# Kernel tuning notes

Measured on AMD Instinct MI355X. Metric: run time of the kernel, lower is better.

## Reference

```python
import jax, jax.numpy as jnp
import numpy as np

D_MODEL, HIDDEN, H, NB = 1024, 128, 16, 32
B, L = 4, 4096


def setup_inputs() -> dict:
    key = jax.random.key(0)
    ks = jax.random.split(key, 6)
    theta_path = jax.random.normal(ks[0], (B, L, H, NB), dtype=jnp.float32)
    content_emb = jax.random.normal(ks[1], (B, L, D_MODEL), dtype=jnp.float32)
    # params (log_Pi init 0.0; final linear weight scaled by 0.01, bias 0, as in torch init)
    log_Pi = jnp.zeros((H, NB), dtype=jnp.float32)
    W1 = jax.random.normal(ks[2], (D_MODEL, HIDDEN), dtype=jnp.float32) / np.sqrt(D_MODEL)
    b1 = jnp.zeros((HIDDEN,), dtype=jnp.float32)
    W2 = (jax.random.normal(ks[3], (HIDDEN, H * NB), dtype=jnp.float32) / np.sqrt(HIDDEN)) * 0.01
    b2 = jnp.zeros((H * NB,), dtype=jnp.float32)
    return {"theta_path": theta_path, "content_emb": content_emb,
            "log_Pi": log_Pi, "W1": W1, "b1": b1, "W2": W2, "b2": b2}


def _affine_combine(c1, c2):
    a1, u1 = c1
    a2, u2 = c2
    return a2 * a1, a2 * u1 + u2


def reference(theta_path, content_emb, log_Pi, W1, b1, W2, b2):
    Bx, Lx, Hx, NBx = theta_path.shape
    # log_R_head: Linear -> GELU(exact) -> Linear, then clamp
    h = jax.nn.gelu(content_emb @ W1 + b1, approximate=False)
    log_R = jnp.clip((h @ W2 + b2).reshape(Bx, Lx, Hx, NBx), -5.0, 5.0)
    R = jnp.exp(log_R)
    # wrapped innovation nu = atan2(sin(-theta), cos(-theta))
    nu = jnp.arctan2(jnp.sin(-theta_path), jnp.cos(-theta_path))
    Pi = jnp.exp(log_Pi)[None, None]            # [1,1,H,NB]
    K = Pi / jnp.maximum(Pi + R, 1e-8)
    alpha = 1.0 - K
    u = K * nu
    # affine recurrence d_t = alpha_t * d_{t-1} + u_t, parallel scan over L
    _, d = jax.lax.associative_scan(_affine_combine, (alpha, u), axis=1)
    return theta_path + d, jnp.broadcast_to(Pi, R.shape), K, R
```

## Files before the change

kernel.cpp:

```cpp
#include <hip/hip_runtime.h>
#include <math.h>

#define B_   4
#define L_   4096
#define C_   512
#define DM_  1024
#define HID_ 128
#define M_   (B_*L_)
#define NC_  256
#define CT_  16

typedef __attribute__((ext_vector_type(8))) short short8;
typedef __attribute__((ext_vector_type(4))) float f32x4;

__device__ __forceinline__ unsigned short f2bf(float f) {
  unsigned u = __float_as_uint(f);
  u += 0x7fffu + ((u >> 16) & 1u);
  return (unsigned short)(u >> 16);
}

__device__ __forceinline__ float wrap_neg(float th) {
  return 6.283185307179586f * rintf(th * 0.15915494309189535f) - th;
}

__global__ __launch_bounds__(256) void k_prep(const float* __restrict__ W1,
                                              const float* __restrict__ W2,
                                              unsigned short* __restrict__ W1T,
                                              unsigned short* __restrict__ W2T) {
  int idx = blockIdx.x * 256 + threadIdx.x;
  if (idx < DM_ * HID_) {
    int n = idx >> 10, k = idx & 1023;
    W1T[idx] = f2bf(W1[(size_t)k * HID_ + n]);
  }
  int i2 = idx - DM_ * HID_;
  if (i2 >= 0 && i2 < HID_ * C_) {
    int n = i2 >> 7, k = i2 & 127;
    W2T[i2] = f2bf(W2[(size_t)k * C_ + n]);
  }
}

__global__ __launch_bounds__(512) void k_mega(const float* __restrict__ X,
                                              const unsigned short* __restrict__ W1T,
                                              const float* __restrict__ b1,
                                              const unsigned short* __restrict__ W2T,
                                              const float* __restrict__ b2,
                                              const float* __restrict__ logPi,
                                              const float* __restrict__ theta,
                                              float* __restrict__ out1,
                                              float* __restrict__ out2,
                                              float* __restrict__ out3,
                                              float* __restrict__ Ab,
                                              float* __restrict__ Ub) {
  __shared__ char lds[49152];
  const int tid  = threadIdx.x;
  const int m0   = blockIdx.x * 32;
  const int lane = tid & 63;
  const int wave = tid >> 6;
  const int wr   = wave >> 2;
  const int wc   = wave & 3;
  const int fr   = lane & 15;
  const int kg   = lane >> 4;

  f32x4 acc[2];
  acc[0] = (f32x4){0.f, 0.f, 0.f, 0.f};
  acc[1] = (f32x4){0.f, 0.f, 0.f, 0.f};

#define STAGE1(bufi, k0)                                                           \
  {                                                                                \
    if (tid < 256) {                                                               \
      int row = tid >> 3, k8 = tid & 7;                                            \
      const f32x4* src = (const f32x4*)(X + (size_t)(m0 + row) * DM_ + (k0) + k8 * 8); \
      f32x4 v0 = __builtin_nontemporal_load(src);                                  \
      f32x4 v1 = __builtin_nontemporal_load(src + 1);                              \
      uint4 pk;                                                                    \
      pk.x = f2bf(v0[0]) | ((unsigned)f2bf(v0[1]) << 16);                          \
      pk.y = f2bf(v0[2]) | ((unsigned)f2bf(v0[3]) << 16);                          \
      pk.z = f2bf(v1[0]) | ((unsigned)f2bf(v1[1]) << 16);                          \
      pk.w = f2bf(v1[2]) | ((unsigned)f2bf(v1[3]) << 16);                          \
      *(uint4*)(lds + (bufi) * 4096 + row * 128 + ((k8 ^ (row & 7)) << 4)) = pk;   \
    }                                                                              \
    _Pragma("unroll")                                                              \
    for (int t = 0; t < 2; ++t) {                                                  \
      int c = tid + t * 512;                                                       \
      int n = c >> 3, k8 = c & 7;                                                  \
      uint4 v = *(const uint4*)(W1T + (size_t)n * DM_ + (k0) + k8 * 8);            \
      *(uint4*)(lds + 8192 + (bufi) * 16384 + n * 128 + ((k8 ^ (n & 7)) << 4)) = v;\
    }                                                                              \
  }

  STAGE1(0, 0);
  __syncthreads();
  for (int it = 0; it < 16; ++it) {
    const int cur = it & 1;
    if (it < 15) STAGE1(1 - cur, (it + 1) * 64);
#pragma unroll
    for (int ks = 0; ks < 2; ++ks) {
      int row = wr * 16 + fr;
      short8 a = *(const short8*)(lds + cur * 4096 + row * 128 +
                                  (((ks * 4 + kg) ^ (row & 7)) << 4));
#pragma unroll
      for (int j = 0; j < 2; ++j) {
        int col = wc * 32 + j * 16 + fr;
        short8 b = *(const short8*)(lds + 8192 + cur * 16384 + col * 128 +
                                    (((ks * 4 + kg) ^ (col & 7)) << 4));
        acc[j] = __builtin_amdgcn_mfma_f32_16x16x32_bf16(a, b, acc[j], 0, 0, 0);
      }
    }
    __syncthreads();
  }
#pragma unroll
  for (int j = 0; j < 2; ++j) {
    int col = wc * 32 + j * 16 + fr;
    float bb = b1[col];
#pragma unroll
    for (int r = 0; r < 4; ++r) {
      int row = wr * 16 + kg * 4 + r;
      float x = acc[j][r] + bb;
      float g = 0.5f * x * (1.0f + erff(x * 0.70710678f));
      *(unsigned short*)(lds + 40960 + row * 256 +
                         (((col >> 3) ^ (row & 15)) << 4) + ((col & 7) << 1)) = f2bf(g);
    }
  }

  const int bidx = m0 >> 12;
  const int ch   = ((m0 & 4095) >> 4) + wr;
  const size_t chbase = ((size_t)(bidx * NC_ + ch)) * C_;

#define STAGE2(bufi, nc)                                                           \
  {                                                                                \
    _Pragma("unroll")                                                              \
    for (int t = 0; t < 2; ++t) {                                                  \
      int c = tid + t * 512;                                                       \
      int n = c >> 4, k8 = c & 15;                                                 \
      uint4 v = *(const uint4*)(W2T + (size_t)((nc) * 64 + n) * HID_ + k8 * 8);    \
      *(uint4*)(lds + (bufi) * 16384 + n * 256 + ((k8 ^ (n & 15)) << 4)) = v;      \
    }                                                                              \
  }

  STAGE2(0, 0);
  __syncthreads();
  for (int nc = 0; nc < 8; ++nc) {
    const int cur = nc & 1;
    if (nc < 7) STAGE2(1 - cur, nc + 1);

    f32x4 a2 = (f32x4){0.f, 0.f, 0.f, 0.f};
#pragma unroll
    for (int ks = 0; ks < 4; ++ks) {
      int row = wr * 16 + fr;
      short8 af = *(const short8*)(lds + 40960 + row * 256 +
                                   (((ks * 4 + kg) ^ (row & 15)) << 4));
      int col = wc * 16 + fr;
      short8 bf2 = *(const short8*)(lds + cur * 16384 + col * 256 +
                                    (((ks * 4 + kg) ^ (col & 15)) << 4));
      a2 = __builtin_amdgcn_mfma_f32_16x16x32_bf16(af, bf2, a2, 0, 0, 0);
    }

    {
      int col = nc * 64 + wc * 16 + fr;
      float Pi = expf(logPi[col]);
      float bb = b2[col];
      float A = 1.f, U = 0.f;
#pragma unroll
      for (int r = 0; r < 4; ++r) {
        int row = m0 + wr * 16 + kg * 4 + r;
        float lr = a2[r] + bb;
        lr = fminf(5.0f, fmaxf(-5.0f, lr));
        float R = expf(lr);
        float K = Pi / fmaxf(Pi + R, 1e-8f);
        size_t o = (size_t)row * C_ + col;
        __builtin_nontemporal_store(Pi, &out1[o]);
        out2[o] = K;
        __builtin_nontemporal_store(R, &out3[o]);
        float nu = wrap_neg(theta[o]);
        float a = 1.f - K;
        U = a * U + K * nu;
        A = a * A;
      }
      float oA = __shfl_xor(A, 16), oU = __shfl_xor(U, 16);
      if ((kg & 1) == 0) { U = oA * U + oU; A = oA * A; }
      else               { U = A * oU + U;  A = A * oA; }
      oA = __shfl_xor(A, 32); oU = __shfl_xor(U, 32);
      if ((kg & 2) == 0) { U = oA * U + oU; A = oA * A; }
      else               { U = A * oU + U;  A = A * oA; }
      if (kg == 0) { Ab[chbase + col] = A; Ub[chbase + col] = U; }
    }
    __syncthreads();
  }
}

__global__ __launch_bounds__(256) void k_scan2(const float* __restrict__ Ab,
                                               const float* __restrict__ Ub,
                                               float* __restrict__ D0) {
  __shared__ float cA[16][17], cU[16][17], carry[16][17];
  const int tid = threadIdx.x;
  const int b   = blockIdx.x >> 5;
  const int c0  = (blockIdx.x & 31) * 16;
  const int c_l = tid & 15, s = tid >> 4;
  const int c   = c0 + c_l;
  float A = 1.f, U = 0.f;
#pragma unroll
  for (int k = 0; k < 16; ++k) {
    size_t o = ((size_t)(b * NC_ + s * 16 + k)) * C_ + c;
    float a = Ab[o], u = Ub[o];
    U = a * U + u; A *= a;
  }
  cA[s][c_l] = A; cU[s][c_l] = U;
  __syncthreads();
  if (tid < 16) {
    float P = 0.f;
#pragma unroll
    for (int ss = 0; ss < 16; ++ss) {
      carry[ss][tid] = P;
      P = cA[ss][tid] * P + cU[ss][tid];
    }
  }
  __syncthreads();
  float d = carry[s][c_l];
#pragma unroll
  for (int k = 0; k < 16; ++k) {
    size_t o = ((size_t)(b * NC_ + s * 16 + k)) * C_ + c;
    D0[o] = d;
    d = Ab[o] * d + Ub[o];
  }
}

__global__ __launch_bounds__(256) void k_scan3(const float* __restrict__ Kv,
                                               const float* __restrict__ theta,
                                               const float* __restrict__ D0,
                                               float* __restrict__ out0) {
  const int b  = blockIdx.x / NC_;
  const int ch = blockIdx.x % NC_;
  const int c  = blockIdx.y * 256 + threadIdx.x;
  size_t base = ((size_t)b * L_ + (size_t)ch * CT_) * C_ + c;
  float d = D0[((size_t)(b * NC_ + ch)) * C_ + c];
#pragma unroll 4
  for (int j = 0; j < CT_; ++j) {
    size_t idx = base + (size_t)j * C_;
    float k  = Kv[idx];
    float th = theta[idx];
    float nu = wrap_neg(th);
    d = (1.f - k) * d + k * nu;
    __builtin_nontemporal_store(th + d, &out0[idx]);
  }
}

extern "C" void kernel_launch(void* const* d_in, const int* in_sizes, int n_in,
                              void* d_out, int out_size, void* d_ws, size_t ws_size,
                              hipStream_t stream) {
  const float* theta = (const float*)d_in[0];
  const float* X     = (const float*)d_in[1];
  const float* logPi = (const float*)d_in[2];
  const float* W1    = (const float*)d_in[3];
  const float* b1    = (const float*)d_in[4];
  const float* W2    = (const float*)d_in[5];
  const float* b2    = (const float*)d_in[6];

  float* out = (float*)d_out;
  const size_t S = (size_t)M_ * C_;
  float* out0 = out;
  float* out1 = out + S;
  float* out2 = out + 2 * S;
  float* out3 = out + 3 * S;

  unsigned short* W1T = (unsigned short*)d_ws;
  unsigned short* W2T = W1T + (size_t)DM_ * HID_;
  float* Ab = (float*)(W2T + (size_t)HID_ * C_);
  float* Ub = Ab + (size_t)B_ * NC_ * C_;
  float* D0 = Ub + (size_t)B_ * NC_ * C_;

  hipLaunchKernelGGL(k_prep, dim3(768), dim3(256), 0, stream, W1, W2, W1T, W2T);
  hipLaunchKernelGGL(k_mega, dim3(M_ / 32), dim3(512), 0, stream,
                     X, W1T, b1, W2T, b2, logPi, theta, out1, out2, out3, Ab, Ub);
  hipLaunchKernelGGL(k_scan2, dim3(B_ * 32), dim3(256), 0, stream, Ab, Ub, D0);
  hipLaunchKernelGGL(k_scan3, dim3(B_ * NC_, 2), dim3(256), 0, stream, out2, theta, D0, out0);
}
```

Measured before the change: 83.25 us.

## Split MLP from epilogue, pass log_R through a quantized 16-bit intermediate

Splits the fused MLP+epilogue kernel into two. The MLP kernel now writes only the clamped log_R, quantized to 16-bit fixed point. A separate epilogue kernel reads it back with coalesced 2-wide vector loads and stores, computes R, K and Pi, and does the per-chunk affine scan serially instead of with cross-lane shuffles. This targets the scattered, poorly coalesced output stores in the MFMA layout. In exchange it adds an extra round trip through global memory, an extra launch, and quantization error in R (step about 1.5e-4 in log space).

```diff
diff --git a/kernel.cpp b/kernel.cpp
--- a/kernel.cpp
+++ b/kernel.cpp
@@ -12,6 +12,7 @@
 
 typedef __attribute__((ext_vector_type(8))) short short8;
 typedef __attribute__((ext_vector_type(4))) float f32x4;
+typedef __attribute__((ext_vector_type(2))) float f32x2;
 
 __device__ __forceinline__ unsigned short f2bf(float f) {
   unsigned u = __float_as_uint(f);
@@ -39,18 +40,12 @@
   }
 }
 
-__global__ __launch_bounds__(512) void k_mega(const float* __restrict__ X,
-                                              const unsigned short* __restrict__ W1T,
-                                              const float* __restrict__ b1,
-                                              const unsigned short* __restrict__ W2T,
-                                              const float* __restrict__ b2,
-                                              const float* __restrict__ logPi,
-                                              const float* __restrict__ theta,
-                                              float* __restrict__ out1,
-                                              float* __restrict__ out2,
-                                              float* __restrict__ out3,
-                                              float* __restrict__ Ab,
-                                              float* __restrict__ Ub) {
+__global__ __launch_bounds__(512) void k_mlp(const float* __restrict__ X,
+                                             const unsigned short* __restrict__ W1T,
+                                             const float* __restrict__ b1,
+                                             const unsigned short* __restrict__ W2T,
+                                             const float* __restrict__ b2,
+                                             unsigned short* __restrict__ logRq) {
   __shared__ char lds[49152];
   const int tid  = threadIdx.x;
   const int m0   = blockIdx.x * 32;
@@ -122,10 +117,6 @@
     }
   }
 
-  const int bidx = m0 >> 12;
-  const int ch   = ((m0 & 4095) >> 4) + wr;
-  const size_t chbase = ((size_t)(bidx * NC_ + ch)) * C_;
-
 #define STAGE2(bufi, nc)                                                           \
   {                                                                                \
     _Pragma("unroll")                                                              \
@@ -154,38 +145,61 @@
                                     (((ks * 4 + kg) ^ (col & 15)) << 4));
       a2 = __builtin_amdgcn_mfma_f32_16x16x32_bf16(af, bf2, a2, 0, 0, 0);
     }
-
     {
       int col = nc * 64 + wc * 16 + fr;
-      float Pi = expf(logPi[col]);
       float bb = b2[col];
-      float A = 1.f, U = 0.f;
 #pragma unroll
       for (int r = 0; r < 4; ++r) {
         int row = m0 + wr * 16 + kg * 4 + r;
         float lr = a2[r] + bb;
         lr = fminf(5.0f, fmaxf(-5.0f, lr));
-        float R = expf(lr);
-        float K = Pi / fmaxf(Pi + R, 1e-8f);
-        size_t o = (size_t)row * C_ + col;
-        __builtin_nontemporal_store(Pi, &out1[o]);
-        out2[o] = K;
-        __builtin_nontemporal_store(R, &out3[o]);
-        float nu = wrap_neg(theta[o]);
-        float a = 1.f - K;
-        U = a * U + K * nu;
-        A = a * A;
+        logRq[(size_t)row * C_ + col] = (unsigned short)rintf((lr + 5.0f) * 6553.5f);
       }
-      float oA = __shfl_xor(A, 16), oU = __shfl_xor(U, 16);
-      if ((kg & 1) == 0) { U = oA * U + oU; A = oA * A; }
-      else               { U = A * oU + U;  A = A * oA; }
-      oA = __shfl_xor(A, 32); oU = __shfl_xor(U, 32);
-      if ((kg & 2) == 0) { U = oA * U + oU; A = oA * A; }
-      else               { U = A * oU + U;  A = A * oA; }
-      if (kg == 0) { Ab[chbase + col] = A; Ub[chbase + col] = U; }
     }
     __syncthreads();
   }
+}
+
+__global__ __launch_bounds__(256) void k_epi(const unsigned short* __restrict__ logRq,
+                                             const float* __restrict__ logPi,
+                                             const float* __restrict__ theta,
+                                             float* __restrict__ out1,
+                                             float* __restrict__ out2,
+                                             float* __restrict__ out3,
+                                             float* __restrict__ Ab,
+                                             float* __restrict__ Ub) {
+  const int blk = blockIdx.x;
+  const int b   = blk >> 8;
+  const int ch  = blk & 255;
+  const int c0  = threadIdx.x * 2;
+  const float Pi0 = expf(logPi[c0]);
+  const float Pi1 = expf(logPi[c0 + 1]);
+  const size_t rowbase = ((size_t)b * L_ + (size_t)ch * CT_) * C_;
+  float A0 = 1.f, U0 = 0.f, A1 = 1.f, U1 = 0.f;
+  const float dq = 1.0f / 6553.5f;
+#pragma unroll
+  for (int j = 0; j < CT_; ++j) {
+    size_t o = rowbase + (size_t)j * C_ + c0;
+    unsigned q = *(const unsigned*)(logRq + o);
+    f32x2 th = *(const f32x2*)(theta + o);
+    float lr0 = (float)(q & 0xffffu) * dq - 5.0f;
+    float lr1 = (float)(q >> 16) * dq - 5.0f;
+    float R0 = expf(lr0), R1 = expf(lr1);
+    float K0 = Pi0 / fmaxf(Pi0 + R0, 1e-8f);
+    float K1 = Pi1 / fmaxf(Pi1 + R1, 1e-8f);
+    f32x2 p2 = {Pi0, Pi1}, k2 = {K0, K1}, r2 = {R0, R1};
+    __builtin_nontemporal_store(p2, (f32x2*)(out1 + o));
+    *(f32x2*)(out2 + o) = k2;
+    __builtin_nontemporal_store(r2, (f32x2*)(out3 + o));
+    float nu0 = wrap_neg(th[0]), nu1 = wrap_neg(th[1]);
+    float a0 = 1.f - K0, a1 = 1.f - K1;
+    U0 = a0 * U0 + K0 * nu0; A0 *= a0;
+    U1 = a1 * U1 + K1 * nu1; A1 *= a1;
+  }
+  size_t co = ((size_t)(b * NC_ + ch)) * C_ + c0;
+  f32x2 A2 = {A0, A1}, U2 = {U0, U1};
+  *(f32x2*)(Ab + co) = A2;
+  *(f32x2*)(Ub + co) = U2;
 }
 
 __global__ __launch_bounds__(256) void k_scan2(const float* __restrict__ Ab,
@@ -262,15 +276,18 @@
   float* out2 = out + 2 * S;
   float* out3 = out + 3 * S;
 
-  unsigned short* W1T = (unsigned short*)d_ws;
-  unsigned short* W2T = W1T + (size_t)DM_ * HID_;
-  float* Ab = (float*)(W2T + (size_t)HID_ * C_);
+  unsigned short* W1T   = (unsigned short*)d_ws;
+  unsigned short* W2T   = W1T + (size_t)DM_ * HID_;
+  unsigned short* logRq = W2T + (size_t)HID_ * C_;
+  float* Ab = (float*)(logRq + S);
   float* Ub = Ab + (size_t)B_ * NC_ * C_;
   float* D0 = Ub + (size_t)B_ * NC_ * C_;
 
   hipLaunchKernelGGL(k_prep, dim3(768), dim3(256), 0, stream, W1, W2, W1T, W2T);
-  hipLaunchKernelGGL(k_mega, dim3(M_ / 32), dim3(512), 0, stream,
-                     X, W1T, b1, W2T, b2, logPi, theta, out1, out2, out3, Ab, Ub);
+  hipLaunchKernelGGL(k_mlp, dim3(M_ / 32), dim3(512), 0, stream,
+                     X, W1T, b1, W2T, b2, logRq);
+  hipLaunchKernelGGL(k_epi, dim3(B_ * NC_), dim3(256), 0, stream,
+                     logRq, logPi, theta, out1, out2, out3, Ab, Ub);
   hipLaunchKernelGGL(k_scan2, dim3(B_ * 32), dim3(256), 0, stream, Ab, Ub, D0);
   hipLaunchKernelGGL(k_scan3, dim3(B_ * NC_, 2), dim3(256), 0, stream, out2, theta, D0, out0);
 }
```

New measurement: 86.85 us. 1.04x slower.

## Load MFMA B-operands from global into registers instead of staging through LDS

Applied to the files above, without the earlier changes.

The fused MLP-plus-scan kernel stops staging W1 and W2 tiles through shared memory. Each wave now loads its own B fragments directly from global memory into registers, double-buffered across iterations, and theta is prefetched one chunk ahead. LDS shrinks from 48KB to about 16.5KB, which could raise occupancy and removes the barriers in the second GEMM loop. The cost is redundant global/L2 reads of the weights across waves and more register pressure.

```diff
diff --git a/kernel.cpp b/kernel.cpp
--- a/kernel.cpp
+++ b/kernel.cpp
@@ -51,7 +51,7 @@
                                               float* __restrict__ out3,
                                               float* __restrict__ Ab,
                                               float* __restrict__ Ub) {
-  __shared__ char lds[49152];
+  __shared__ char lds[16896];
   const int tid  = threadIdx.x;
   const int m0   = blockIdx.x * 32;
   const int lane = tid & 63;
@@ -61,130 +61,146 @@
   const int fr   = lane & 15;
   const int kg   = lane >> 4;
 
-  f32x4 acc[2];
-  acc[0] = (f32x4){0.f, 0.f, 0.f, 0.f};
-  acc[1] = (f32x4){0.f, 0.f, 0.f, 0.f};
-
-#define STAGE1(bufi, k0)                                                           \
-  {                                                                                \
-    if (tid < 256) {                                                               \
-      int row = tid >> 3, k8 = tid & 7;                                            \
-      const f32x4* src = (const f32x4*)(X + (size_t)(m0 + row) * DM_ + (k0) + k8 * 8); \
-      f32x4 v0 = __builtin_nontemporal_load(src);                                  \
-      f32x4 v1 = __builtin_nontemporal_load(src + 1);                              \
-      uint4 pk;                                                                    \
-      pk.x = f2bf(v0[0]) | ((unsigned)f2bf(v0[1]) << 16);                          \
-      pk.y = f2bf(v0[2]) | ((unsigned)f2bf(v0[3]) << 16);                          \
-      pk.z = f2bf(v1[0]) | ((unsigned)f2bf(v1[1]) << 16);                          \
-      pk.w = f2bf(v1[2]) | ((unsigned)f2bf(v1[3]) << 16);                          \
-      *(uint4*)(lds + (bufi) * 4096 + row * 128 + ((k8 ^ (row & 7)) << 4)) = pk;   \
-    }                                                                              \
-    _Pragma("unroll")                                                              \
-    for (int t = 0; t < 2; ++t) {                                                  \
-      int c = tid + t * 512;                                                       \
-      int n = c >> 3, k8 = c & 7;                                                  \
-      uint4 v = *(const uint4*)(W1T + (size_t)n * DM_ + (k0) + k8 * 8);            \
-      *(uint4*)(lds + 8192 + (bufi) * 16384 + n * 128 + ((k8 ^ (n & 7)) << 4)) = v;\
-    }                                                                              \
-  }
-
-  STAGE1(0, 0);
-  __syncthreads();
+  const int srow = tid >> 4;
+  const int sk4  = tid & 15;
+  const float* xsrc = X + (size_t)(m0 + srow) * DM_ + sk4 * 4;
+  char* swr = lds + srow * 128 + ((sk4 << 3) ^ ((srow & 7) << 4));
+
+  const unsigned short* w1p0 = W1T + (size_t)(wc * 32 + fr) * DM_ + kg * 8;
+  const unsigned short* w1p1 = W1T + (size_t)(wc * 32 + 16 + fr) * DM_ + kg * 8;
+
+  f32x4 acc0 = {0.f, 0.f, 0.f, 0.f};
+  f32x4 acc1 = {0.f, 0.f, 0.f, 0.f};
+
+  {
+    f32x4 xv = __builtin_nontemporal_load((const f32x4*)xsrc);
+    unsigned p0 = f2bf(xv[0]) | ((unsigned)f2bf(xv[1]) << 16);
+    unsigned p1 = f2bf(xv[2]) | ((unsigned)f2bf(xv[3]) << 16);
+    uint2 pk = {p0, p1};
+    *(uint2*)swr = pk;
+  }
+  __syncthreads();
+
+  short8 bc[4], bn[4];
+  bc[0] = *(const short8*)(w1p0);
+  bc[1] = *(const short8*)(w1p1);
+  bc[2] = *(const short8*)(w1p0 + 32);
+  bc[3] = *(const short8*)(w1p1 + 32);
+
+  const int arow = wr * 16 + fr;
+  char* ard = lds + arow * 128;
+
   for (int it = 0; it < 16; ++it) {
     const int cur = it & 1;
-    if (it < 15) STAGE1(1 - cur, (it + 1) * 64);
+    f32x4 xv;
+    if (it < 15) {
+      xv = __builtin_nontemporal_load((const f32x4*)(xsrc + (it + 1) * 64));
+      const unsigned short* p0 = w1p0 + (it + 1) * 64;
+      const unsigned short* p1 = w1p1 + (it + 1) * 64;
+      bn[0] = *(const short8*)(p0);
+      bn[1] = *(const short8*)(p1);
+      bn[2] = *(const short8*)(p0 + 32);
+      bn[3] = *(const short8*)(p1 + 32);
+    }
 #pragma unroll
     for (int ks = 0; ks < 2; ++ks) {
-      int row = wr * 16 + fr;
-      short8 a = *(const short8*)(lds + cur * 4096 + row * 128 +
-                                  (((ks * 4 + kg) ^ (row & 7)) << 4));
-#pragma unroll
-      for (int j = 0; j < 2; ++j) {
-        int col = wc * 32 + j * 16 + fr;
-        short8 b = *(const short8*)(lds + 8192 + cur * 16384 + col * 128 +
-                                    (((ks * 4 + kg) ^ (col & 7)) << 4));
-        acc[j] = __builtin_amdgcn_mfma_f32_16x16x32_bf16(a, b, acc[j], 0, 0, 0);
-      }
-    }
-    __syncthreads();
-  }
+      short8 a = *(const short8*)(ard + cur * 4096 +
+                                  (((ks * 4 + kg) << 4) ^ ((arow & 7) << 4)));
+      acc0 = __builtin_amdgcn_mfma_f32_16x16x32_bf16(a, bc[ks * 2 + 0], acc0, 0, 0, 0);
+      acc1 = __builtin_amdgcn_mfma_f32_16x16x32_bf16(a, bc[ks * 2 + 1], acc1, 0, 0, 0);
+    }
+    if (it < 15) {
+      unsigned p0 = f2bf(xv[0]) | ((unsigned)f2bf(xv[1]) << 16);
+      unsigned p1 = f2bf(xv[2]) | ((unsigned)f2bf(xv[3]) << 16);
+      uint2 pk = {p0, p1};
+      *(uint2*)(swr + (1 - cur) * 4096) = pk;
+      __syncthreads();
+#pragma unroll
+      for (int q = 0; q < 4; ++q) bc[q] = bn[q];
+    }
+  }
+
 #pragma unroll
   for (int j = 0; j < 2; ++j) {
     int col = wc * 32 + j * 16 + fr;
     float bb = b1[col];
+    f32x4 av = (j == 0) ? acc0 : acc1;
 #pragma unroll
     for (int r = 0; r < 4; ++r) {
       int row = wr * 16 + kg * 4 + r;
-      float x = acc[j][r] + bb;
+      float x = av[r] + bb;
       float g = 0.5f * x * (1.0f + erff(x * 0.70710678f));
-      *(unsigned short*)(lds + 40960 + row * 256 +
-                         (((col >> 3) ^ (row & 15)) << 4) + ((col & 7) << 1)) = f2bf(g);
-    }
-  }
-
-  const int bidx = m0 >> 12;
+      *(unsigned short*)(lds + 8192 + row * 272 + col * 2) = f2bf(g);
+    }
+  }
+  __syncthreads();
+
+  const int bidx = blockIdx.x >> 7;
   const int ch   = ((m0 & 4095) >> 4) + wr;
   const size_t chbase = ((size_t)(bidx * NC_ + ch)) * C_;
-
-#define STAGE2(bufi, nc)                                                           \
-  {                                                                                \
-    _Pragma("unroll")                                                              \
-    for (int t = 0; t < 2; ++t) {                                                  \
-      int c = tid + t * 512;                                                       \
-      int n = c >> 4, k8 = c & 15;                                                 \
-      uint4 v = *(const uint4*)(W2T + (size_t)((nc) * 64 + n) * HID_ + k8 * 8);    \
-      *(uint4*)(lds + (bufi) * 16384 + n * 256 + ((k8 ^ (n & 15)) << 4)) = v;      \
-    }                                                                              \
-  }
-
-  STAGE2(0, 0);
-  __syncthreads();
+  const int colbase = wc * 16 + fr;
+  const unsigned short* w2p = W2T + (size_t)colbase * HID_ + kg * 8;
+  const char* hrd = lds + 8192 + (wr * 16 + fr) * 272;
+  const size_t throw0 = (size_t)(m0 + wr * 16 + kg * 4) * C_;
+
+  short8 c2[4], n2[4];
+#pragma unroll
+  for (int ks = 0; ks < 4; ++ks) c2[ks] = *(const short8*)(w2p + ks * 32);
+  float thc[4], thn[4];
+#pragma unroll
+  for (int r = 0; r < 4; ++r) thc[r] = theta[throw0 + (size_t)r * C_ + colbase];
+
   for (int nc = 0; nc < 8; ++nc) {
-    const int cur = nc & 1;
-    if (nc < 7) STAGE2(1 - cur, nc + 1);
-
-    f32x4 a2 = (f32x4){0.f, 0.f, 0.f, 0.f};
+    const int col = nc * 64 + colbase;
+    if (nc < 7) {
+#pragma unroll
+      for (int ks = 0; ks < 4; ++ks)
+        n2[ks] = *(const short8*)(w2p + (size_t)(nc + 1) * 64 * HID_ + ks * 32);
+#pragma unroll
+      for (int r = 0; r < 4; ++r)
+        thn[r] = theta[throw0 + (size_t)r * C_ + col + 64];
+    }
+    float Pi = expf(logPi[col]);
+    float bb = b2[col];
+
+    f32x4 a2 = {0.f, 0.f, 0.f, 0.f};
 #pragma unroll
     for (int ks = 0; ks < 4; ++ks) {
-      int row = wr * 16 + fr;
-      short8 af = *(const short8*)(lds + 40960 + row * 256 +
-                                   (((ks * 4 + kg) ^ (row & 15)) << 4));
-      int col = wc * 16 + fr;
-      short8 bf2 = *(const short8*)(lds + cur * 16384 + col * 256 +
-                                    (((ks * 4 + kg) ^ (col & 15)) << 4));
-      a2 = __builtin_amdgcn_mfma_f32_16x16x32_bf16(af, bf2, a2, 0, 0, 0);
-    }
-
-    {
-      int col = nc * 64 + wc * 16 + fr;
-      float Pi = expf(logPi[col]);
-      float bb = b2[col];
-      float A = 1.f, U = 0.f;
-#pragma unroll
-      for (int r = 0; r < 4; ++r) {
-        int row = m0 + wr * 16 + kg * 4 + r;
-        float lr = a2[r] + bb;
-        lr = fminf(5.0f, fmaxf(-5.0f, lr));
-        float R = expf(lr);
-        float K = Pi / fmaxf(Pi + R, 1e-8f);
-        size_t o = (size_t)row * C_ + col;
-        __builtin_nontemporal_store(Pi, &out1[o]);
-        out2[o] = K;
-        __builtin_nontemporal_store(R, &out3[o]);
-        float nu = wrap_neg(theta[o]);
-        float a = 1.f - K;
-        U = a * U + K * nu;
-        A = a * A;
-      }
-      float oA = __shfl_xor(A, 16), oU = __shfl_xor(U, 16);
-      if ((kg & 1) == 0) { U = oA * U + oU; A = oA * A; }
-      else               { U = A * oU + U;  A = A * oA; }
-      oA = __shfl_xor(A, 32); oU = __shfl_xor(U, 32);
-      if ((kg & 2) == 0) { U = oA * U + oU; A = oA * A; }
-      else               { U = A * oU + U;  A = A * oA; }
-      if (kg == 0) { Ab[chbase + col] = A; Ub[chbase + col] = U; }
-    }
-    __syncthreads();
+      short8 a = *(const short8*)(hrd + ks * 64 + kg * 16);
+      a2 = __builtin_amdgcn_mfma_f32_16x16x32_bf16(a, c2[ks], a2, 0, 0, 0);
+    }
+
+    float A = 1.f, U = 0.f;
+#pragma unroll
+    for (int r = 0; r < 4; ++r) {
+      int row = m0 + wr * 16 + kg * 4 + r;
+      float lr = a2[r] + bb;
+      lr = fminf(5.0f, fmaxf(-5.0f, lr));
+      float R = expf(lr);
+      float K = Pi / fmaxf(Pi + R, 1e-8f);
+      size_t o = (size_t)row * C_ + col;
+      __builtin_nontemporal_store(Pi, &out1[o]);
+      out2[o] = K;
+      __builtin_nontemporal_store(R, &out3[o]);
+      float nu = wrap_neg(thc[r]);
+      float a = 1.f - K;
+      U = a * U + K * nu;
+      A = a * A;
+    }
+    float oA = __shfl_xor(A, 16), oU = __shfl_xor(U, 16);
+    if ((kg & 1) == 0) { U = oA * U + oU; A = oA * A; }
+    else               { U = A * oU + U;  A = A * oA; }
+    oA = __shfl_xor(A, 32); oU = __shfl_xor(U, 32);
+    if ((kg & 2) == 0) { U = oA * U + oU; A = oA * A; }
+    else               { U = A * oU + U;  A = A * oA; }
+    if (kg == 0) { Ab[chbase + col] = A; Ub[chbase + col] = U; }
+
+    if (nc < 7) {
+#pragma unroll
+      for (int ks = 0; ks < 4; ++ks) c2[ks] = n2[ks];
+#pragma unroll
+      for (int r = 0; r < 4; ++r) thc[r] = thn[r];
+    }
   }
 }
 
```

Result: slower. 89.23 us (+7.2%).
